# Kernel optimization log

Measured on AMD Instinct MI355X. Metric: run time of the kernel, lower is better.

## Reference

```python
import jax, jax.numpy as jnp
import numpy as np

N = 50000      # nodes
E = 800000     # edges (avg degree 16)
D = 64         # emb_dim
L = 5          # num_layer
BN_EPS = 1e-5


def setup_inputs() -> dict:
    key = jax.random.key(0)
    ks = jax.random.split(key, 10)
    x = jax.random.randint(ks[0], (N,), 0, 1)                      # indices into 1-row embedding
    edge_index = jax.random.randint(ks[1], (2, E), 0, N)
    edge_attr = jax.random.normal(ks[2], (E, 7), dtype=jnp.float32)
    s = lambda k, shape: (jax.random.normal(k, shape, dtype=jnp.float32) * 0.05)
    node_emb = s(ks[3], (1, D))
    # per-layer GINConv params, stacked on a leading layer axis for lax.scan
    We = s(ks[4], (L, 7, D));   be = jnp.zeros((L, D), jnp.float32)      # edge_encoder
    eps = jnp.zeros((L,), jnp.float32)                                   # GIN eps
    W1 = s(ks[5], (L, D, 2 * D)); b1 = jnp.zeros((L, 2 * D), jnp.float32)  # mlp linear1
    g1 = jnp.ones((L, 2 * D), jnp.float32); bb1 = jnp.zeros((L, 2 * D), jnp.float32)  # mlp BN
    W2 = s(ks[6], (L, 2 * D, D)); b2 = jnp.zeros((L, D), jnp.float32)    # mlp linear2
    g2 = jnp.ones((L, D), jnp.float32); bb2 = jnp.zeros((L, D), jnp.float32)  # outer BN
    return dict(x=x, edge_index=edge_index, edge_attr=edge_attr, node_emb=node_emb,
                We=We, be=be, eps=eps, W1=W1, b1=b1, g1=g1, bb1=bb1,
                W2=W2, b2=b2, g2=g2, bb2=bb2)


def _bn(a, g, b):
    # BatchNorm1d in training mode: batch statistics over node axis, biased var
    m = a.mean(axis=0)
    v = jnp.var(a, axis=0)
    return (a - m) * jax.lax.rsqrt(v + BN_EPS) * g + b


def reference(x, edge_index, edge_attr, node_emb, We, be, eps,
              W1, b1, g1, bb1, W2, b2, g2, bb2):
    src, dst = edge_index[0], edge_index[1]
    h = node_emb[x]                                    # [N, D]
    relu_flags = jnp.arange(L) < (L - 1)               # ReLU on all but last layer

    def step(h, p):
        We_, be_, eps_, W1_, b1_, g1_, bb1_, W2_, b2_, g2_, bb2_, flag = p
        ee = edge_attr @ We_ + be_                     # [E, D] edge embeddings
        msg = jax.nn.relu(h[src] + ee)                 # gather + elementwise
        agg = jax.ops.segment_sum(msg, dst, num_segments=N)  # scatter-add
        z = (1.0 + eps_) * h + agg                     # GIN combine
        a = jax.nn.relu(_bn(z @ W1_ + b1_, g1_, bb1_)) # mlp: lin -> BN -> ReLU
        hb = _bn(a @ W2_ + b2_, g2_, bb2_)             # lin -> outer BN
        h_new = jnp.where(flag, jax.nn.relu(hb), hb)   # dropout omitted (eval)
        return h_new, None

    h, _ = jax.lax.scan(step, h, (We, be, eps, W1, b1, g1, bb1, W2, b2, g2, bb2, relu_flags))
    return h                                           # JK='last'
```

## Files before the change

kernel.cpp:

```cpp
#include <hip/hip_runtime.h>
#include <hip/hip_fp16.h>

#define NN 50000
#define EE 800000
#define NB 782
#define NBKT 196
#define BCAP 4608
#define PSLOT 6144

typedef _Float16 f16x8 __attribute__((ext_vector_type(8)));
typedef _Float16 f16x2 __attribute__((ext_vector_type(2)));
typedef float f32x4 __attribute__((ext_vector_type(4)));

__device__ __forceinline__ unsigned h2u(__half2 h) {
    union { __half2 h; unsigned u; } c; c.h = h; return c.u;
}
__device__ __forceinline__ f16x2 u2h(unsigned u) {
    union { unsigned u; f16x2 h; } c; c.u = u; return c.h;
}

__global__ __launch_bounds__(256) void bin_kernel(
    const int* __restrict__ ei, const float* __restrict__ ea,
    int* __restrict__ bktcur, int4* __restrict__ srec,
    unsigned short* __restrict__ sdst)
{
    __shared__ int cnt[NBKT], base[NBKT];
    const int t = threadIdx.x;
    if (t < NBKT) cnt[t] = 0;
    __syncthreads();
    const int e0 = blockIdx.x << 12;
    int meta[16];
#pragma unroll
    for (int j = 0; j < 16; ++j) {
        const int e = e0 + (j << 8) + t;
        if (e < EE) {
            const int d = ei[EE + e];
            const int bk = d >> 8;
            const int rk = atomicAdd(&cnt[bk], 1);
            meta[j] = (rk << 16) | (bk << 8) | (d & 255);
        } else meta[j] = -1;
    }
    __syncthreads();
    if (t < NBKT) base[t] = cnt[t] ? atomicAdd(&bktcur[t], cnt[t]) : 0;
    __syncthreads();
#pragma unroll
    for (int j = 0; j < 16; ++j) {
        if (meta[j] < 0) continue;
        const int bk = (meta[j] >> 8) & 255;
        const int slot = base[bk] + (meta[j] >> 16);
        if (slot >= BCAP) continue;
        const int pos = bk * BCAP + slot;
        const int e = e0 + (j << 8) + t;
        const int src = ei[e];
        const float* a = ea + e * 7;
        const unsigned h0 = __half_as_ushort(__float2half(a[0]));
        const unsigned h1 = __half_as_ushort(__float2half(a[1]));
        const unsigned h2 = __half_as_ushort(__float2half(a[2]));
        const unsigned h3 = __half_as_ushort(__float2half(a[3]));
        const unsigned h4 = __half_as_ushort(__float2half(a[4]));
        const unsigned h5 = __half_as_ushort(__float2half(a[5]));
        const unsigned h6 = __half_as_ushort(__float2half(a[6]));
        srec[pos] = make_int4((int)(h0 | (h1 << 16)), (int)(h2 | (h3 << 16)),
                              (int)(h4 | (h5 << 16)), (int)(h6 | ((unsigned)src << 16)));
        sdst[pos] = (unsigned short)(meta[j] & 255);
    }
}

__global__ __launch_bounds__(256) void buildB_kernel(
    const int* __restrict__ bktcur, const int4* __restrict__ srec,
    const unsigned short* __restrict__ sdst,
    int2* __restrict__ offSE, int4* __restrict__ pea)
{
    __shared__ int nc[256], sm[256], curs[256];
    const int b = blockIdx.x, t = threadIdx.x;
    nc[t] = 0;
    __syncthreads();
    const int nE = min(bktcur[b], BCAP);
    const int sb = b * BCAP;
    for (int i = t; i < nE; i += 256) atomicAdd(&nc[(int)sdst[sb + i]], 1);
    __syncthreads();
    const int node = (b << 8) + t;
    const int used = nc[t];
    const int pd = (node < NN) ? ((used + 7) & ~7) : 0;
    sm[t] = pd;
    __syncthreads();
    for (int o = 1; o < 256; o <<= 1) {
        const int u = (t >= o) ? sm[t - o] : 0;
        __syncthreads();
        sm[t] += u;
        __syncthreads();
    }
    const int st = b * PSLOT + sm[t] - pd;
    if (node < NN) offSE[node] = make_int2(st, st + pd);
    curs[t] = st;
    __syncthreads();
    for (int i = t; i < nE; i += 256) {
        const int ln = (int)sdst[sb + i];
        const int p = atomicAdd(&curs[ln], 1);
        pea[p] = srec[sb + i];
    }
    __syncthreads();
    if (node < NN) {
        const int end = st + pd;
        for (int p = curs[t]; p < end; ++p)
            pea[p] = make_int4(0, 0, 0, (int)(((unsigned)NN) << 16));
    }
}

__global__ __launch_bounds__(256) void prep_kernel(
    const int* __restrict__ x, const float* __restrict__ nemb,
    __half* __restrict__ h16, unsigned* __restrict__ z32,
    const float* __restrict__ W1, const float* __restrict__ W2,
    const float* __restrict__ We, const float* __restrict__ be,
    _Float16* __restrict__ W1s, _Float16* __restrict__ W2s,
    unsigned* __restrict__ Wepk, unsigned* __restrict__ be2)
{
    if (blockIdx.x < 3125) {
        const int i4 = (blockIdx.x << 8) + threadIdx.x;
        if (blockIdx.x == 0 && threadIdx.x < 32)
            ((unsigned*)h16)[(NN << 5) + threadIdx.x] = 0xFBFFFBFFu;
        if (i4 < 1536) z32[1600000 + i4] = 0u;
        const int n = i4 >> 4;
        const float4 v = ((const float4*)nemb)[(x[n] << 4) + (i4 & 15)];
        *(int2*)(h16 + (i4 << 2)) =
            make_int2((int)h2u(__floats2half2_rn(v.x, v.y)),
                      (int)h2u(__floats2half2_rn(v.z, v.w)));
        return;
    }
    const int i = ((blockIdx.x - 3125) << 8) + threadIdx.x;
    if (i < 40960) {
        const int l = i >> 13, j = i & 8191, k = j >> 7, n = j & 127;
        W1s[(l << 13) + ((((k >> 3) << 7) + n) << 3) + (k & 7)] = (_Float16)W1[i];
    } else if (i < 81920) {
        const int i2 = i - 40960;
        const int l = i2 >> 13, j = i2 & 8191, k = j >> 6, n = j & 63;
        W2s[(l << 13) + ((((k >> 3) << 6) + n) << 3) + (k & 7)] = (_Float16)W2[i2];
    } else if (i < 83040) {
        const int i3 = i - 81920;
        const int l = i3 / 224;
        const int r = i3 - l * 224;
        const int k = r >> 5, s = r & 31;
        const float* W = We + l * 448 + (k << 6) + (s << 1);
        Wepk[i3] = h2u(__floats2half2_rn(W[0], W[1]));
    } else if (i < 83200) {
        const int i4 = i - 83040;
        const int l = i4 >> 5, s = i4 & 31;
        const float* B = be + (l << 6) + (s << 1);
        be2[i4] = h2u(__floats2half2_rn(B[0], B[1]));
    }
}

__global__ __launch_bounds__(256) void hprep_kernel(
    const float* __restrict__ y2, const float* __restrict__ acc2,
    const float* __restrict__ g2p, const float* __restrict__ bb2p,
    __half* __restrict__ h16)
{
    __shared__ float scshL[128];
    const int t = threadIdx.x;
    if (t < 64) {
        float ss = 0.f, qq = 0.f;
#pragma unroll
        for (int c = 0; c < 8; ++c) {
            ss += acc2[(c << 7) + t];
            qq += acc2[(c << 7) + 64 + t];
        }
        const float m = ss * (1.0f / NN);
        const float v = fmaxf(qq * (1.0f / NN) - m * m, 0.0f);
        const float sc = g2p[t] * rsqrtf(v + 1e-5f);
        scshL[t] = sc;
        scshL[64 + t] = bb2p[t] - m * sc;
    }
    __syncthreads();
    const int i4 = (blockIdx.x << 8) + t;
    const float4 v = ((const float4*)y2)[i4];
    const int d0 = (i4 << 2) & 63;
    const float a = fmaxf(fmaf(v.x, scshL[d0 + 0], scshL[64 + d0 + 0]), 0.f);
    const float b = fmaxf(fmaf(v.y, scshL[d0 + 1], scshL[64 + d0 + 1]), 0.f);
    const float c = fmaxf(fmaf(v.z, scshL[d0 + 2], scshL[64 + d0 + 2]), 0.f);
    const float d = fmaxf(fmaf(v.w, scshL[d0 + 3], scshL[64 + d0 + 3]), 0.f);
    *(int2*)(h16 + (i4 << 2)) =
        make_int2((int)h2u(__floats2half2_rn(a, b)),
                  (int)h2u(__floats2half2_rn(c, d)));
}

__global__ __launch_bounds__(256) void gather_kernel(
    const int2* __restrict__ offSE, const int4* __restrict__ pea,
    const unsigned* __restrict__ h32,
    const unsigned* __restrict__ Wepk, const unsigned* __restrict__ be2,
    const float* __restrict__ epsp,
    unsigned* __restrict__ z32)
{
    const int t = threadIdx.x;
    const int lane = t & 63;
    const int s = lane & 31;
    const int n = (blockIdx.x << 3) + ((t >> 6) << 1) + (lane >> 5);

    const f16x2 w0 = u2h(Wepk[s]),       w1 = u2h(Wepk[32 + s]),
                w2 = u2h(Wepk[64 + s]),  w3 = u2h(Wepk[96 + s]),
                w4 = u2h(Wepk[128 + s]), w5 = u2h(Wepk[160 + s]),
                w6 = u2h(Wepk[192 + s]);
    const f16x2 beh = u2h(be2[s]);

    const int2 se = offSE[n];
    const int e0 = se.x, e1 = se.y;

    f16x2 acc2 = (f16x2){(_Float16)0.f, (_Float16)0.f};
    int e = e0;
    if (((e1 - e0) >> 3) & 1) {
        int4 pk[8];
#pragma unroll
        for (int j = 0; j < 8; ++j) pk[j] = pea[e + j];
        unsigned hv[8];
#pragma unroll
        for (int j = 0; j < 8; ++j)
            hv[j] = h32[(((int)(((unsigned)pk[j].w) >> 16)) << 5) + s];
#pragma unroll
        for (int j = 0; j < 8; ++j) {
            const f16x2 a01 = u2h((unsigned)pk[j].x);
            const f16x2 a23 = u2h((unsigned)pk[j].y);
            const f16x2 a45 = u2h((unsigned)pk[j].z);
            const f16x2 a6x = u2h((unsigned)pk[j].w);
            f16x2 ee = beh;
            ee += (f16x2){a01[0], a01[0]} * w0;
            ee += (f16x2){a01[1], a01[1]} * w1;
            ee += (f16x2){a23[0], a23[0]} * w2;
            ee += (f16x2){a23[1], a23[1]} * w3;
            ee += (f16x2){a45[0], a45[0]} * w4;
            ee += (f16x2){a45[1], a45[1]} * w5;
            ee += (f16x2){a6x[0], a6x[0]} * w6;
            f16x2 m2 = u2h(hv[j]) + ee;
            const _Float16 zz = (_Float16)0.f;
            m2 = (f16x2){ m2[0] > zz ? m2[0] : zz, m2[1] > zz ? m2[1] : zz };
            acc2 += m2;
        }
        e += 8;
    }
    for (; e < e1; e += 16) {
        int4 pk[16];
#pragma unroll
        for (int j = 0; j < 16; ++j) pk[j] = pea[e + j];
        unsigned hv[16];
#pragma unroll
        for (int j = 0; j < 16; ++j)
            hv[j] = h32[(((int)(((unsigned)pk[j].w) >> 16)) << 5) + s];
#pragma unroll
        for (int j = 0; j < 16; ++j) {
            const f16x2 a01 = u2h((unsigned)pk[j].x);
            const f16x2 a23 = u2h((unsigned)pk[j].y);
            const f16x2 a45 = u2h((unsigned)pk[j].z);
            const f16x2 a6x = u2h((unsigned)pk[j].w);
            f16x2 ee = beh;
            ee += (f16x2){a01[0], a01[0]} * w0;
            ee += (f16x2){a01[1], a01[1]} * w1;
            ee += (f16x2){a23[0], a23[0]} * w2;
            ee += (f16x2){a23[1], a23[1]} * w3;
            ee += (f16x2){a45[0], a45[0]} * w4;
            ee += (f16x2){a45[1], a45[1]} * w5;
            ee += (f16x2){a6x[0], a6x[0]} * w6;
            f16x2 m2 = u2h(hv[j]) + ee;
            const _Float16 zz = (_Float16)0.f;
            m2 = (f16x2){ m2[0] > zz ? m2[0] : zz, m2[1] > zz ? m2[1] : zz };
            acc2 += m2;
        }
    }
    const f16x2 hn2 = u2h(h32[(n << 5) + s]);
    const float e1f = 1.0f + epsp[0];
    const float zLo = fmaf(e1f, (float)hn2[0], (float)acc2[0]);
    const float zHi = fmaf(e1f, (float)hn2[1], (float)acc2[1]);
    z32[(n << 5) + s] = h2u(__floats2half2_rn(zLo, zHi));
}

__global__ __launch_bounds__(256) void mm1_kernel(
    const _Float16* __restrict__ z16, const _Float16* __restrict__ W1s,
    const float* __restrict__ b1p, _Float16* __restrict__ y1h,
    float* __restrict__ acc1)
{
    __shared__ float smS[4][128], smQ[4][128];
    const int t = threadIdx.x;
    const int wv = t >> 6, lane = t & 63;
    const int q = lane >> 4, ln = lane & 15;
    const int r0 = blockIdx.x << 6;

    const int rowm = r0 + (wv << 4) + ln;
    const f16x8 af0 = *(const f16x8*)(z16 + rowm * 64 + (q << 3));
    const f16x8 af1 = *(const f16x8*)(z16 + rowm * 64 + 32 + (q << 3));

    f32x4 acc[8];
#pragma unroll
    for (int n0 = 0; n0 < 8; ++n0) acc[n0] = (f32x4){0.f, 0.f, 0.f, 0.f};
#pragma unroll
    for (int n0 = 0; n0 < 8; ++n0) {
        const f16x8 bf0 = *(const f16x8*)(W1s + (((q << 7) + (n0 << 4) + ln) << 3));
        const f16x8 bf1 = *(const f16x8*)(W1s + ((((4 + q) << 7) + (n0 << 4) + ln) << 3));
        acc[n0] = __builtin_amdgcn_mfma_f32_16x16x32_f16(af0, bf0, acc[n0], 0, 0, 0);
        acc[n0] = __builtin_amdgcn_mfma_f32_16x16x32_f16(af1, bf1, acc[n0], 0, 0, 0);
    }

    const int baseRow = r0 + (wv << 4) + (q << 2);
#pragma unroll
    for (int n0 = 0; n0 < 8; ++n0) {
        const int col = (n0 << 4) + ln;
        const float bb = b1p[col];
        float s = 0.f, sq = 0.f;
#pragma unroll
        for (int rg = 0; rg < 4; ++rg) {
            const int row = baseRow + rg;
            const float y = acc[n0][rg] + bb;
            y1h[row * 128 + col] = (_Float16)y;
            const float m = (row < NN) ? 1.f : 0.f;
            s = fmaf(m, y, s); sq = fmaf(m, y * y, sq);
        }
        s += __shfl_xor(s, 16); s += __shfl_xor(s, 32);
        sq += __shfl_xor(sq, 16); sq += __shfl_xor(sq, 32);
        if (lane < 16) { smS[wv][col] = s; smQ[wv][col] = sq; }
    }
    __syncthreads();
    if (t < 128) {
        const float s4 = smS[0][t] + smS[1][t] + smS[2][t] + smS[3][t];
        const float q4 = smQ[0][t] + smQ[1][t] + smQ[2][t] + smQ[3][t];
        float* a1 = acc1 + ((blockIdx.x & 7) << 8);
        atomicAdd(&a1[t], s4);
        atomicAdd(&a1[128 + t], q4);
    }
}

__global__ __launch_bounds__(256) void mm2_kernel(
    const _Float16* __restrict__ y1h, const float* __restrict__ acc1,
    const float* __restrict__ g1p, const float* __restrict__ bb1p,
    const _Float16* __restrict__ W2s, const float* __restrict__ b2,
    float* __restrict__ y2, float* __restrict__ acc2)
{
    __shared__ float smS[4][64], smQ[4][64];
    __shared__ float scshL[256];
    const int t = threadIdx.x;
    const int wv = t >> 6, lane = t & 63;
    const int q = lane >> 4, ln = lane & 15;
    const int r0 = blockIdx.x << 6;

    if (t < 128) {
        float ss = 0.f, qq = 0.f;
#pragma unroll
        for (int c = 0; c < 8; ++c) {
            ss += acc1[(c << 8) + t];
            qq += acc1[(c << 8) + 128 + t];
        }
        const float m = ss * (1.0f / NN);
        const float v = fmaxf(qq * (1.0f / NN) - m * m, 0.0f);
        const float sc = g1p[t] * rsqrtf(v + 1e-5f);
        scshL[t] = sc;
        scshL[128 + t] = bb1p[t] - m * sc;
    }
    __syncthreads();

    const int rowm = r0 + (wv << 4) + ln;
    f16x8 af[4];
#pragma unroll
    for (int ks = 0; ks < 4; ++ks) {
        const int k0 = (ks << 5) + (q << 3);
        const f16x8 raw = *(const f16x8*)(y1h + rowm * 128 + k0);
        f16x8 a;
#pragma unroll
        for (int j = 0; j < 8; ++j) {
            const float sc = scshL[k0 + j], sh = scshL[128 + k0 + j];
            a[j] = (_Float16)fmaxf(fmaf((float)raw[j], sc, sh), 0.f);
        }
        af[ks] = a;
    }

    f32x4 acc[4];
#pragma unroll
    for (int n0 = 0; n0 < 4; ++n0) acc[n0] = (f32x4){0.f, 0.f, 0.f, 0.f};
#pragma unroll
    for (int n0 = 0; n0 < 4; ++n0) {
#pragma unroll
        for (int ks = 0; ks < 4; ++ks) {
            const f16x8 bf = *(const f16x8*)(
                W2s + (((((ks << 2) + q) << 6) + (n0 << 4) + ln) << 3));
            acc[n0] = __builtin_amdgcn_mfma_f32_16x16x32_f16(af[ks], bf, acc[n0], 0, 0, 0);
        }
    }

    const int baseRow = r0 + (wv << 4) + (q << 2);
#pragma unroll
    for (int n0 = 0; n0 < 4; ++n0) {
        const int col = (n0 << 4) + ln;
        const float bb = b2[col];
        float sa = 0.f, sq = 0.f;
#pragma unroll
        for (int rg = 0; rg < 4; ++rg) {
            const int row = baseRow + rg;
            const float y = acc[n0][rg] + bb;
            y2[row * 64 + col] = y;
            const float m = (row < NN) ? 1.f : 0.f;
            sa = fmaf(m, y, sa); sq = fmaf(m, y * y, sq);
        }
        sa += __shfl_xor(sa, 16); sa += __shfl_xor(sa, 32);
        sq += __shfl_xor(sq, 16); sq += __shfl_xor(sq, 32);
        if (lane < 16) { smS[wv][col] = sa; smQ[wv][col] = sq; }
    }
    __syncthreads();
    if (t < 64) {
        const float s4 = smS[0][t] + smS[1][t] + smS[2][t] + smS[3][t];
        const float q4 = smQ[0][t] + smQ[1][t] + smQ[2][t] + smQ[3][t];
        float* a2 = acc2 + ((blockIdx.x & 7) << 7);
        atomicAdd(&a2[t], s4);
        atomicAdd(&a2[64 + t], q4);
    }
}

__global__ __launch_bounds__(256) void final_kernel(
    const float* __restrict__ y2, const float* __restrict__ acc2,
    const float* __restrict__ g2p, const float* __restrict__ bb2p,
    float* __restrict__ out)
{
    __shared__ float scshL[128];
    const int t = threadIdx.x;
    if (t < 64) {
        float ss = 0.f, qq = 0.f;
#pragma unroll
        for (int c = 0; c < 8; ++c) {
            ss += acc2[(c << 7) + t];
            qq += acc2[(c << 7) + 64 + t];
        }
        const float m = ss * (1.0f / NN);
        const float v = fmaxf(qq * (1.0f / NN) - m * m, 0.0f);
        const float sc = g2p[t] * rsqrtf(v + 1e-5f);
        scshL[t] = sc;
        scshL[64 + t] = bb2p[t] - m * sc;
    }
    __syncthreads();
    const int i4 = (blockIdx.x << 8) + t;
    const float4 v = ((const float4*)y2)[i4];
    const int d0 = (i4 << 2) & 63;
    float4 o;
    o.x = fmaf(v.x, scshL[d0 + 0], scshL[64 + d0 + 0]);
    o.y = fmaf(v.y, scshL[d0 + 1], scshL[64 + d0 + 1]);
    o.z = fmaf(v.z, scshL[d0 + 2], scshL[64 + d0 + 2]);
    o.w = fmaf(v.w, scshL[d0 + 3], scshL[64 + d0 + 3]);
    ((float4*)out)[i4] = o;
}

extern "C" void kernel_launch(void* const* d_in, const int* in_sizes, int n_in,
                              void* d_out, int out_size, void* d_ws, size_t ws_size,
                              hipStream_t stream)
{
    const int*   x    = (const int*)d_in[0];
    const int*   ei   = (const int*)d_in[1];
    const float* ea   = (const float*)d_in[2];
    const float* nemb = (const float*)d_in[3];
    const float* We   = (const float*)d_in[4];
    const float* be   = (const float*)d_in[5];
    const float* eps  = (const float*)d_in[6];
    const float* W1   = (const float*)d_in[7];
    const float* b1   = (const float*)d_in[8];
    const float* g1   = (const float*)d_in[9];
    const float* bb1  = (const float*)d_in[10];
    const float* W2   = (const float*)d_in[11];
    const float* b2   = (const float*)d_in[12];
    const float* g2   = (const float*)d_in[13];
    const float* bb2  = (const float*)d_in[14];
    float* out = (float*)d_out;

    int*      iws   = (int*)d_ws;
    float*    fws   = (float*)d_ws;
    int2*     offSE = (int2*)iws;
    int*      bktcur= iws + 100096;
    float*    accbuf= fws + 100352;
    _Float16* W1s   = (_Float16*)(fws + 115712);
    _Float16* W2s   = (_Float16*)(fws + 136192);
    unsigned* Wepk  = (unsigned*)(fws + 156672);
    unsigned* be2   = (unsigned*)(fws + 157792);
    int4*     pea   = (int4*)(iws + 157952);
    _Float16* z16   = (_Float16*)(fws + 4974848);
    _Float16* y1h   = (_Float16*)(fws + 6576384);
    float*    y2    = fws + 6576384;
    __half*   h16   = (__half*)(fws + 9779456);

    int4*           srec = (int4*)(fws + 4974848);
    unsigned short* sdst = (unsigned short*)(fws + 9779456);

    hipMemsetAsync(bktcur, 0, (115712 - 100096) * sizeof(int), stream);

    bin_kernel   <<<196,  256, 0, stream>>>(ei, ea, bktcur, srec, sdst);
    buildB_kernel<<<NBKT, 256, 0, stream>>>(bktcur, srec, sdst, offSE, pea);
    prep_kernel  <<<3450, 256, 0, stream>>>(x, nemb, h16, (unsigned*)z16,
                                            W1, W2, We, be, W1s, W2s, Wepk, be2);

    for (int l = 0; l < 5; ++l) {
        float* acc1 = accbuf + l * 3072;
        float* acc2 = accbuf + l * 3072 + 2048;

        gather_kernel<<<6250, 256, 0, stream>>>(
            offSE, pea, (const unsigned*)h16, Wepk + l * 224, be2 + l * 32,
            eps + l, (unsigned*)z16);

        mm1_kernel<<<NB, 256, 0, stream>>>(z16, W1s + l * 8192, b1 + l * 128,
                                           y1h, acc1);

        mm2_kernel<<<NB, 256, 0, stream>>>(y1h, acc1, g1 + l * 128, bb1 + l * 128,
                                           W2s + l * 8192, b2 + l * 64, y2, acc2);

        if (l < 4)
            hprep_kernel<<<3125, 256, 0, stream>>>(y2, acc2, g2 + l * 64,
                                                   bb2 + l * 64, h16);
    }

    final_kernel<<<3125, 256, 0, stream>>>(y2, accbuf + 4 * 3072 + 2048,
                                           g2 + 4 * 64, bb2 + 4 * 64, out);
}
```

Before: 408.9 us.

## Merge build and prep kernels, store y2 in fp16, accumulate gather in fp32

```diff
diff --git a/kernel.cpp b/kernel.cpp
--- a/kernel.cpp
+++ b/kernel.cpp
@@ -66,48 +66,10 @@
     }
 }
 
-__global__ __launch_bounds__(256) void buildB_kernel(
+__global__ __launch_bounds__(256) void buildprep_kernel(
     const int* __restrict__ bktcur, const int4* __restrict__ srec,
     const unsigned short* __restrict__ sdst,
-    int2* __restrict__ offSE, int4* __restrict__ pea)
-{
-    __shared__ int nc[256], sm[256], curs[256];
-    const int b = blockIdx.x, t = threadIdx.x;
-    nc[t] = 0;
-    __syncthreads();
-    const int nE = min(bktcur[b], BCAP);
-    const int sb = b * BCAP;
-    for (int i = t; i < nE; i += 256) atomicAdd(&nc[(int)sdst[sb + i]], 1);
-    __syncthreads();
-    const int node = (b << 8) + t;
-    const int used = nc[t];
-    const int pd = (node < NN) ? ((used + 7) & ~7) : 0;
-    sm[t] = pd;
-    __syncthreads();
-    for (int o = 1; o < 256; o <<= 1) {
-        const int u = (t >= o) ? sm[t - o] : 0;
-        __syncthreads();
-        sm[t] += u;
-        __syncthreads();
-    }
-    const int st = b * PSLOT + sm[t] - pd;
-    if (node < NN) offSE[node] = make_int2(st, st + pd);
-    curs[t] = st;
-    __syncthreads();
-    for (int i = t; i < nE; i += 256) {
-        const int ln = (int)sdst[sb + i];
-        const int p = atomicAdd(&curs[ln], 1);
-        pea[p] = srec[sb + i];
-    }
-    __syncthreads();
-    if (node < NN) {
-        const int end = st + pd;
-        for (int p = curs[t]; p < end; ++p)
-            pea[p] = make_int4(0, 0, 0, (int)(((unsigned)NN) << 16));
-    }
-}
-
-__global__ __launch_bounds__(256) void prep_kernel(
+    int2* __restrict__ offSE, int4* __restrict__ pea,
     const int* __restrict__ x, const float* __restrict__ nemb,
     __half* __restrict__ h16, unsigned* __restrict__ z32,
     const float* __restrict__ W1, const float* __restrict__ W2,
@@ -115,10 +77,49 @@
     _Float16* __restrict__ W1s, _Float16* __restrict__ W2s,
     unsigned* __restrict__ Wepk, unsigned* __restrict__ be2)
 {
-    if (blockIdx.x < 3125) {
-        const int i4 = (blockIdx.x << 8) + threadIdx.x;
-        if (blockIdx.x == 0 && threadIdx.x < 32)
-            ((unsigned*)h16)[(NN << 5) + threadIdx.x] = 0xFBFFFBFFu;
+    const int t = threadIdx.x;
+    if (blockIdx.x < NBKT) {
+        __shared__ int nc[256], sm[256], curs[256];
+        const int b = blockIdx.x;
+        nc[t] = 0;
+        __syncthreads();
+        const int nE = min(bktcur[b], BCAP);
+        const int sb = b * BCAP;
+        for (int i = t; i < nE; i += 256) atomicAdd(&nc[(int)sdst[sb + i]], 1);
+        __syncthreads();
+        const int node = (b << 8) + t;
+        const int used = nc[t];
+        const int pd = (node < NN) ? ((used + 7) & ~7) : 0;
+        sm[t] = pd;
+        __syncthreads();
+        for (int o = 1; o < 256; o <<= 1) {
+            const int u = (t >= o) ? sm[t - o] : 0;
+            __syncthreads();
+            sm[t] += u;
+            __syncthreads();
+        }
+        const int st = b * PSLOT + sm[t] - pd;
+        if (node < NN) offSE[node] = make_int2(st, st + pd);
+        curs[t] = st;
+        __syncthreads();
+        for (int i = t; i < nE; i += 256) {
+            const int ln = (int)sdst[sb + i];
+            const int p = atomicAdd(&curs[ln], 1);
+            pea[p] = srec[sb + i];
+        }
+        __syncthreads();
+        if (node < NN) {
+            const int end = st + pd;
+            for (int p = curs[t]; p < end; ++p)
+                pea[p] = make_int4(0, 0, 0, (int)(((unsigned)NN) << 16));
+        }
+        return;
+    }
+    const int pb = blockIdx.x - NBKT;
+    if (pb < 3125) {
+        const int i4 = (pb << 8) + t;
+        if (pb == 0 && t < 32)
+            ((unsigned*)h16)[(NN << 5) + t] = 0xFBFFFBFFu;
         if (i4 < 1536) z32[1600000 + i4] = 0u;
         const int n = i4 >> 4;
         const float4 v = ((const float4*)nemb)[(x[n] << 4) + (i4 & 15)];
@@ -127,7 +128,7 @@
                       (int)h2u(__floats2half2_rn(v.z, v.w)));
         return;
     }
-    const int i = ((blockIdx.x - 3125) << 8) + threadIdx.x;
+    const int i = ((pb - 3125) << 8) + t;
     if (i < 40960) {
         const int l = i >> 13, j = i & 8191, k = j >> 7, n = j & 127;
         W1s[(l << 13) + ((((k >> 3) << 7) + n) << 3) + (k & 7)] = (_Float16)W1[i];
@@ -151,7 +152,7 @@
 }
 
 __global__ __launch_bounds__(256) void hprep_kernel(
-    const float* __restrict__ y2, const float* __restrict__ acc2,
+    const _Float16* __restrict__ y2h, const float* __restrict__ acc2,
     const float* __restrict__ g2p, const float* __restrict__ bb2p,
     __half* __restrict__ h16)
 {
@@ -172,12 +173,13 @@
     }
     __syncthreads();
     const int i4 = (blockIdx.x << 8) + t;
-    const float4 v = ((const float4*)y2)[i4];
+    const int2 v = ((const int2*)y2h)[i4];
+    const f16x2 ab = u2h((unsigned)v.x), cd = u2h((unsigned)v.y);
     const int d0 = (i4 << 2) & 63;
-    const float a = fmaxf(fmaf(v.x, scshL[d0 + 0], scshL[64 + d0 + 0]), 0.f);
-    const float b = fmaxf(fmaf(v.y, scshL[d0 + 1], scshL[64 + d0 + 1]), 0.f);
-    const float c = fmaxf(fmaf(v.z, scshL[d0 + 2], scshL[64 + d0 + 2]), 0.f);
-    const float d = fmaxf(fmaf(v.w, scshL[d0 + 3], scshL[64 + d0 + 3]), 0.f);
+    const float a = fmaxf(fmaf((float)ab[0], scshL[d0 + 0], scshL[64 + d0 + 0]), 0.f);
+    const float b = fmaxf(fmaf((float)ab[1], scshL[d0 + 1], scshL[64 + d0 + 1]), 0.f);
+    const float c = fmaxf(fmaf((float)cd[0], scshL[d0 + 2], scshL[64 + d0 + 2]), 0.f);
+    const float d = fmaxf(fmaf((float)cd[1], scshL[d0 + 3], scshL[64 + d0 + 3]), 0.f);
     *(int2*)(h16 + (i4 << 2)) =
         make_int2((int)h2u(__floats2half2_rn(a, b)),
                   (int)h2u(__floats2half2_rn(c, d)));
@@ -204,7 +206,7 @@
     const int2 se = offSE[n];
     const int e0 = se.x, e1 = se.y;
 
-    f16x2 acc2 = (f16x2){(_Float16)0.f, (_Float16)0.f};
+    float accLo = 0.f, accHi = 0.f;
     int e = e0;
     if (((e1 - e0) >> 3) & 1) {
         int4 pk[8];
@@ -228,10 +230,9 @@
             ee += (f16x2){a45[0], a45[0]} * w4;
             ee += (f16x2){a45[1], a45[1]} * w5;
             ee += (f16x2){a6x[0], a6x[0]} * w6;
-            f16x2 m2 = u2h(hv[j]) + ee;
-            const _Float16 zz = (_Float16)0.f;
-            m2 = (f16x2){ m2[0] > zz ? m2[0] : zz, m2[1] > zz ? m2[1] : zz };
-            acc2 += m2;
+            const f16x2 hh2 = u2h(hv[j]);
+            accLo += fmaxf((float)hh2[0] + (float)ee[0], 0.f);
+            accHi += fmaxf((float)hh2[1] + (float)ee[1], 0.f);
         }
         e += 8;
     }
@@ -257,16 +258,15 @@
             ee += (f16x2){a45[0], a45[0]} * w4;
             ee += (f16x2){a45[1], a45[1]} * w5;
             ee += (f16x2){a6x[0], a6x[0]} * w6;
-            f16x2 m2 = u2h(hv[j]) + ee;
-            const _Float16 zz = (_Float16)0.f;
-            m2 = (f16x2){ m2[0] > zz ? m2[0] : zz, m2[1] > zz ? m2[1] : zz };
-            acc2 += m2;
+            const f16x2 hh2 = u2h(hv[j]);
+            accLo += fmaxf((float)hh2[0] + (float)ee[0], 0.f);
+            accHi += fmaxf((float)hh2[1] + (float)ee[1], 0.f);
         }
     }
     const f16x2 hn2 = u2h(h32[(n << 5) + s]);
     const float e1f = 1.0f + epsp[0];
-    const float zLo = fmaf(e1f, (float)hn2[0], (float)acc2[0]);
-    const float zHi = fmaf(e1f, (float)hn2[1], (float)acc2[1]);
+    const float zLo = fmaf(e1f, (float)hn2[0], accLo);
+    const float zHi = fmaf(e1f, (float)hn2[1], accHi);
     z32[(n << 5) + s] = h2u(__floats2half2_rn(zLo, zHi));
 }
 
@@ -328,7 +328,7 @@
     const _Float16* __restrict__ y1h, const float* __restrict__ acc1,
     const float* __restrict__ g1p, const float* __restrict__ bb1p,
     const _Float16* __restrict__ W2s, const float* __restrict__ b2,
-    float* __restrict__ y2, float* __restrict__ acc2)
+    _Float16* __restrict__ y2h, float* __restrict__ acc2)
 {
     __shared__ float smS[4][64], smQ[4][64];
     __shared__ float scshL[256];
@@ -390,7 +390,7 @@
         for (int rg = 0; rg < 4; ++rg) {
             const int row = baseRow + rg;
             const float y = acc[n0][rg] + bb;
-            y2[row * 64 + col] = y;
+            y2h[row * 64 + col] = (_Float16)y;
             const float m = (row < NN) ? 1.f : 0.f;
             sa = fmaf(m, y, sa); sq = fmaf(m, y * y, sq);
         }
@@ -409,7 +409,7 @@
 }
 
 __global__ __launch_bounds__(256) void final_kernel(
-    const float* __restrict__ y2, const float* __restrict__ acc2,
+    const _Float16* __restrict__ y2h, const float* __restrict__ acc2,
     const float* __restrict__ g2p, const float* __restrict__ bb2p,
     float* __restrict__ out)
 {
@@ -430,13 +430,14 @@
     }
     __syncthreads();
     const int i4 = (blockIdx.x << 8) + t;
-    const float4 v = ((const float4*)y2)[i4];
+    const int2 v = ((const int2*)y2h)[i4];
+    const f16x2 ab = u2h((unsigned)v.x), cd = u2h((unsigned)v.y);
     const int d0 = (i4 << 2) & 63;
     float4 o;
-    o.x = fmaf(v.x, scshL[d0 + 0], scshL[64 + d0 + 0]);
-    o.y = fmaf(v.y, scshL[d0 + 1], scshL[64 + d0 + 1]);
-    o.z = fmaf(v.z, scshL[d0 + 2], scshL[64 + d0 + 2]);
-    o.w = fmaf(v.w, scshL[d0 + 3], scshL[64 + d0 + 3]);
+    o.x = fmaf((float)ab[0], scshL[d0 + 0], scshL[64 + d0 + 0]);
+    o.y = fmaf((float)ab[1], scshL[d0 + 1], scshL[64 + d0 + 1]);
+    o.z = fmaf((float)cd[0], scshL[d0 + 2], scshL[64 + d0 + 2]);
+    o.w = fmaf((float)cd[1], scshL[d0 + 3], scshL[64 + d0 + 3]);
     ((float4*)out)[i4] = o;
 }
 
@@ -473,18 +474,17 @@
     int4*     pea   = (int4*)(iws + 157952);
     _Float16* z16   = (_Float16*)(fws + 4974848);
     _Float16* y1h   = (_Float16*)(fws + 6576384);
-    float*    y2    = fws + 6576384;
-    __half*   h16   = (__half*)(fws + 9779456);
-
-    int4*           srec = (int4*)(fws + 4974848);
-    unsigned short* sdst = (unsigned short*)(fws + 9779456);
+    _Float16* y2h   = (_Float16*)(fws + 9779456);
+    __half*   h16   = (__half*)(fws + 11380992);
+    int4*           srec = (int4*)(fws + 12981056);
+    unsigned short* sdst = (unsigned short*)(fws + 16593728);
 
     hipMemsetAsync(bktcur, 0, (115712 - 100096) * sizeof(int), stream);
 
-    bin_kernel   <<<196,  256, 0, stream>>>(ei, ea, bktcur, srec, sdst);
-    buildB_kernel<<<NBKT, 256, 0, stream>>>(bktcur, srec, sdst, offSE, pea);
-    prep_kernel  <<<3450, 256, 0, stream>>>(x, nemb, h16, (unsigned*)z16,
-                                            W1, W2, We, be, W1s, W2s, Wepk, be2);
+    bin_kernel      <<<196,  256, 0, stream>>>(ei, ea, bktcur, srec, sdst);
+    buildprep_kernel<<<3646, 256, 0, stream>>>(
+        bktcur, srec, sdst, offSE, pea, x, nemb, h16, (unsigned*)z16,
+        W1, W2, We, be, W1s, W2s, Wepk, be2);
 
     for (int l = 0; l < 5; ++l) {
         float* acc1 = accbuf + l * 3072;
@@ -498,13 +498,13 @@
                                            y1h, acc1);
 
         mm2_kernel<<<NB, 256, 0, stream>>>(y1h, acc1, g1 + l * 128, bb1 + l * 128,
-                                           W2s + l * 8192, b2 + l * 64, y2, acc2);
+                                           W2s + l * 8192, b2 + l * 64, y2h, acc2);
 
         if (l < 4)
-            hprep_kernel<<<3125, 256, 0, stream>>>(y2, acc2, g2 + l * 64,
+            hprep_kernel<<<3125, 256, 0, stream>>>(y2h, acc2, g2 + l * 64,
                                                    bb2 + l * 64, h16);
     }
 
-    final_kernel<<<3125, 256, 0, stream>>>(y2, accbuf + 4 * 3072 + 2048,
+    final_kernel<<<3125, 256, 0, stream>>>(y2h, accbuf + 4 * 3072 + 2048,
                                            g2 + 4 * 64, bb2 + 4 * 64, out);
 }
```

Result: no change. 409.1 us (+0.0%).
